# Optimization experiments

Measured on AMD Instinct MI355X. Metric: run time of the kernel, lower is better.

The kernel has to match this reference:

```python
import jax, jax.numpy as jnp
import numpy as np

N_T, N_I = 4096, 4096
TEXT_DIM, IMAGE_DIM, HIDDEN_DIM = 1024, 1024, 1024


def setup_inputs() -> dict:
    key = jax.random.key(0)
    ks = jax.random.split(key, 8)
    s_t = 1.0 / np.sqrt(TEXT_DIM)
    s_i = 1.0 / np.sqrt(IMAGE_DIM)
    return {
        "text_features": jax.random.normal(ks[0], (N_T, TEXT_DIM), jnp.float32),
        "image_features": jax.random.normal(ks[1], (N_I, IMAGE_DIM), jnp.float32),
        # nn.Linear params: weight [out, in], bias [out]
        "w_text": jax.random.uniform(ks[2], (HIDDEN_DIM, TEXT_DIM), jnp.float32, -s_t, s_t),
        "b_text": jax.random.uniform(ks[3], (HIDDEN_DIM,), jnp.float32, -s_t, s_t),
        "w_image": jax.random.uniform(ks[4], (HIDDEN_DIM, IMAGE_DIM), jnp.float32, -s_i, s_i),
        "b_image": jax.random.uniform(ks[5], (HIDDEN_DIM,), jnp.float32, -s_i, s_i),
        "scale_TI": jnp.ones((1,), jnp.float32),
        "scale_IT": jnp.ones((1,), jnp.float32),
    }


def reference(text_features, image_features, w_text, b_text, w_image, b_image, scale_TI, scale_IT):
    # linear projections to shared hidden space
    t = text_features @ w_text.T + b_text      # [N_t, H]
    i = image_features @ w_image.T + b_image   # [N_i, H]
    inv_sqrt_h = 1.0 / jnp.sqrt(jnp.asarray(HIDDEN_DIM, t.dtype))
    # text -> image attention: softmax over image axis, scaled post-softmax
    logits_TI = (t @ i.T) * inv_sqrt_h               # [N_t, N_i]
    attn_TI = jax.nn.softmax(logits_TI, axis=-1) * scale_TI
    # image -> text attention
    attn_IT = jax.nn.softmax(logits_TI.T, axis=-1) * scale_IT  # [N_i, N_t]
    text_attention_on_image = attn_TI @ image_features  # [N_t, image_dim]
    image_attention_on_text = attn_IT @ text_features   # [N_i, text_dim]
    return (text_attention_on_image, image_attention_on_text)
```

## Files before the change

kernel.cpp:

```cpp
#include <hip/hip_runtime.h>


typedef __bf16 bf16x8 __attribute__((ext_vector_type(8)));
typedef float f32x4 __attribute__((ext_vector_type(4)));

#define N_T 4096
#define N_I 4096
#define DIM 1024
#define TSS 136

__device__ __forceinline__ unsigned short f2bf(float f) {
    unsigned int u = __float_as_uint(f);
    u += 0x7fffu + ((u >> 16) & 1u);
    return (unsigned short)(u >> 16);
}

__device__ __forceinline__ void async_cp16(const unsigned short* g, unsigned short* l) {
    __builtin_amdgcn_global_load_lds(
        (const __attribute__((address_space(1))) unsigned int*)g,
        (__attribute__((address_space(3))) unsigned int*)l, 16, 0, 0);
}

__device__ __forceinline__ void stage_async(const unsigned short* __restrict__ src,
                                            int ld, int row0, int k0,
                                            unsigned short* lds, int t) {
    int r = t >> 2, c = (t & 3) << 3;
    const unsigned short* g = src + (size_t)(row0 + r) * ld + k0 + c;
    async_cp16(g, lds + r * 32 + c);
    async_cp16(g + (size_t)64 * ld, lds + (64 + r) * 32 + c);
}

__device__ __forceinline__ void mfma_step(const unsigned short* As,
                                          const unsigned short* Bs, f32x4 acc[4][4],
                                          int wrow, int wcol, int lane16, int quad) {
    bf16x8 a[4], b[4];
#pragma unroll
    for (int i = 0; i < 4; ++i) {
        a[i] = *(const bf16x8*)&As[(wrow + i * 16 + lane16) * 32 + quad * 8];
        b[i] = *(const bf16x8*)&Bs[(wcol + i * 16 + lane16) * 32 + quad * 8];
    }
#pragma unroll
    for (int i = 0; i < 4; ++i)
#pragma unroll
        for (int j = 0; j < 4; ++j)
            acc[i][j] = __builtin_amdgcn_mfma_f32_16x16x32_bf16(a[i], b[j], acc[i][j], 0, 0, 0);
}

__device__ __forceinline__ void tile_store(const unsigned short* sm,
                                           unsigned short* __restrict__ g, int ld,
                                           int row0, int col0, int tid) {
    int r = tid >> 1, h = (tid & 1) << 6;
    const unsigned short* src = sm + r * TSS + h;
    unsigned short* dst = g + (size_t)(row0 + r) * ld + col0 + h;
#pragma unroll
    for (int v = 0; v < 8; ++v)
        *(uint4*)(dst + v * 8) = *(const uint4*)(src + v * 8);
}

#define GEMM_IDX()                                               \
    int tid = threadIdx.x;                                       \
    int m0 = blockIdx.x * 128, n0 = blockIdx.y * 128;            \
    int lane = tid & 63, wave = tid >> 6;                        \
    int lane16 = lane & 15, quad = lane >> 4;                    \
    int wrow = (wave >> 1) * 64, wcol = (wave & 1) * 64;         \
    f32x4 acc[4][4];                                             \
    {                                                            \
        f32x4 z = {0.f, 0.f, 0.f, 0.f};                          \
        for (int i = 0; i < 4; ++i)                              \
            for (int j = 0; j < 4; ++j) acc[i][j] = z;           \
    }

__global__ void __launch_bounds__(256)
cvt_bf16_all(const float* __restrict__ t, const float* __restrict__ im,
             const float* __restrict__ wt, const float* __restrict__ wi,
             unsigned short* __restrict__ tb, unsigned short* __restrict__ imb,
             unsigned short* __restrict__ wtb, unsigned short* __restrict__ wib) {
    size_t i = (size_t)(blockIdx.x * 256 + threadIdx.x) * 8;
    const float* s;
    unsigned short* d;
    size_t off;
    if (i < 4194304)       { s = t;  d = tb;  off = i; }
    else if (i < 8388608)  { s = im; d = imb; off = i - 4194304; }
    else if (i < 9437184)  { s = wt; d = wtb; off = i - 8388608; }
    else                   { s = wi; d = wib; off = i - 9437184; }
    float4 f0 = *(const float4*)(s + off);
    float4 f1 = *(const float4*)(s + off + 4);
    uint4 o;
    o.x = (unsigned int)f2bf(f0.x) | ((unsigned int)f2bf(f0.y) << 16);
    o.y = (unsigned int)f2bf(f0.z) | ((unsigned int)f2bf(f0.w) << 16);
    o.z = (unsigned int)f2bf(f1.x) | ((unsigned int)f2bf(f1.y) << 16);
    o.w = (unsigned int)f2bf(f1.z) | ((unsigned int)f2bf(f1.w) << 16);
    *(uint4*)(d + off) = o;
}

__global__ void __launch_bounds__(256)
transpose_cvt2(const float* __restrict__ im, const float* __restrict__ tx,
               unsigned short* __restrict__ imgT, unsigned short* __restrict__ textT) {
    const float* in = blockIdx.z ? tx : im;
    unsigned short* out = blockIdx.z ? textT : imgT;
    __shared__ float tile[32][33];
    int c0 = blockIdx.x * 32, r0 = blockIdx.y * 32;
    int txi = threadIdx.x & 31, tyi = threadIdx.x >> 5;
#pragma unroll
    for (int i = tyi; i < 32; i += 8)
        tile[i][txi] = in[(size_t)(r0 + i) * DIM + c0 + txi];
    __syncthreads();
#pragma unroll
    for (int i = tyi; i < 32; i += 8)
        out[(size_t)(c0 + i) * N_T + r0 + txi] = f2bf(tile[txi][i]);
}

__global__ void __launch_bounds__(256, 2)
gemm_proj2(const unsigned short* __restrict__ Atx, const unsigned short* __restrict__ Wtx,
           const float* __restrict__ btx, unsigned short* __restrict__ Ctx,
           const unsigned short* __restrict__ Aim, const unsigned short* __restrict__ Wim,
           const float* __restrict__ bim, unsigned short* __restrict__ Cim) {
    __shared__ unsigned short As[128 * 32];
    __shared__ unsigned short Bs[128 * 32];
    int z = blockIdx.z;
    const unsigned short* A = z ? Aim : Atx;
    const unsigned short* W = z ? Wim : Wtx;
    const float* bias = z ? bim : btx;
    unsigned short* C = z ? Cim : Ctx;
    GEMM_IDX();
    for (int k0 = 0; k0 < DIM; k0 += 32) {
        stage_async(A, DIM, m0, k0, As, tid);
        stage_async(W, DIM, n0, k0, Bs, tid);
        __syncthreads();
        mfma_step(As, Bs, acc, wrow, wcol, lane16, quad);
        __syncthreads();
    }
#pragma unroll
    for (int j = 0; j < 4; ++j) {
        int col = n0 + wcol + j * 16 + lane16;
        float bv = bias[col];
#pragma unroll
        for (int i = 0; i < 4; ++i) {
            int rowb = m0 + wrow + i * 16 + quad * 4;
#pragma unroll
            for (int r = 0; r < 4; ++r)
                C[(size_t)(rowb + r) * DIM + col] = f2bf(acc[i][j][r] + bv);
        }
    }
}

__global__ void __launch_bounds__(256, 2)
gemm_logits_exp(const unsigned short* __restrict__ Tb,
                const unsigned short* __restrict__ Ib,
                unsigned short* __restrict__ P, unsigned short* __restrict__ PT,
                float* __restrict__ lT, float* __restrict__ lI) {
    __shared__ unsigned short smem[128 * TSS];
    unsigned short* As = smem;
    unsigned short* Bs = smem + 128 * 32;
    GEMM_IDX();
    for (int k0 = 0; k0 < DIM; k0 += 32) {
        stage_async(Tb, DIM, m0, k0, As, tid);
        stage_async(Ib, DIM, n0, k0, Bs, tid);
        __syncthreads();
        mfma_step(As, Bs, acc, wrow, wcol, lane16, quad);
        __syncthreads();
    }
#pragma unroll
    for (int i = 0; i < 4; ++i)
#pragma unroll
        for (int j = 0; j < 4; ++j)
#pragma unroll
            for (int r = 0; r < 4; ++r)
                acc[i][j][r] = __expf(acc[i][j][r] * 0.03125f);
#pragma unroll
    for (int i = 0; i < 4; ++i)
#pragma unroll
        for (int r = 0; r < 4; ++r) {
            float s = acc[i][0][r] + acc[i][1][r] + acc[i][2][r] + acc[i][3][r];
            s += __shfl_xor(s, 1); s += __shfl_xor(s, 2);
            s += __shfl_xor(s, 4); s += __shfl_xor(s, 8);
            if (lane16 == 0) atomicAdd(&lT[m0 + wrow + i * 16 + quad * 4 + r], s);
        }
#pragma unroll
    for (int j = 0; j < 4; ++j) {
        float s = 0.f;
#pragma unroll
        for (int i = 0; i < 4; ++i)
#pragma unroll
            for (int r = 0; r < 4; ++r) s += acc[i][j][r];
        s += __shfl_xor(s, 16); s += __shfl_xor(s, 32);
        if (quad == 0) atomicAdd(&lI[n0 + wcol + j * 16 + lane16], s);
    }
    __syncthreads();
#pragma unroll
    for (int i = 0; i < 4; ++i)
#pragma unroll
        for (int j = 0; j < 4; ++j)
#pragma unroll
            for (int r = 0; r < 4; ++r)
                smem[(wrow + i * 16 + quad * 4 + r) * TSS + wcol + j * 16 + lane16] =
                    f2bf(acc[i][j][r]);
    __syncthreads();
    tile_store(smem, P, N_I, m0, n0, tid);
    __syncthreads();
#pragma unroll
    for (int i = 0; i < 4; ++i)
#pragma unroll
        for (int j = 0; j < 4; ++j) {
            unsigned int lo = (unsigned int)f2bf(acc[i][j][0]) |
                              ((unsigned int)f2bf(acc[i][j][1]) << 16);
            unsigned int hi = (unsigned int)f2bf(acc[i][j][2]) |
                              ((unsigned int)f2bf(acc[i][j][3]) << 16);
            uint2 v; v.x = lo; v.y = hi;
            *(uint2*)&smem[(wcol + j * 16 + lane16) * TSS + wrow + i * 16 + quad * 4] = v;
        }
    __syncthreads();
    tile_store(smem, PT, N_T, n0, m0, tid);
}

__global__ void __launch_bounds__(512, 4)
gemm_attn2(const unsigned short* __restrict__ P, const unsigned short* __restrict__ imgT,
           const float* __restrict__ lT, const float* __restrict__ sTI,
           float* __restrict__ out0,
           const unsigned short* __restrict__ PT, const unsigned short* __restrict__ textT,
           const float* __restrict__ lI, const float* __restrict__ sIT,
           float* __restrict__ out1) {
    __shared__ unsigned short As[2][128 * 32];
    __shared__ unsigned short Bs[2][128 * 32];
    int which = blockIdx.z;
    const unsigned short* A = which ? PT : P;
    const unsigned short* Bt = which ? textT : imgT;
    const float* l = which ? lI : lT;
    const float* sp = which ? sIT : sTI;
    float* out = which ? out1 : out0;

    int tid = threadIdx.x;
    int half = tid >> 8;
    int t = tid & 255;
    int m0 = blockIdx.x * 128, n0 = blockIdx.y * 128;
    int lane = tid & 63;
    int wv = (tid >> 6) & 3;
    int lane16 = lane & 15, quad = lane >> 4;
    int wrow = (wv >> 1) * 64, wcol = (wv & 1) * 64;
    f32x4 acc[4][4];
    {
        f32x4 z = {0.f, 0.f, 0.f, 0.f};
        for (int i = 0; i < 4; ++i)
            for (int j = 0; j < 4; ++j) acc[i][j] = z;
    }

    int kbeg = half * 2048, kend = kbeg + 2048;
    for (int k0 = kbeg; k0 < kend; k0 += 32) {
        stage_async(A, 4096, m0, k0, As[half], t);
        stage_async(Bt, 4096, n0, k0, Bs[half], t);
        __syncthreads();
        mfma_step(As[half], Bs[half], acc, wrow, wcol, lane16, quad);
        __syncthreads();
    }

    float* red = (float*)As;
#pragma unroll
    for (int i = 0; i < 4; ++i) {
        __syncthreads();
        if (half) {
#pragma unroll
            for (int j = 0; j < 4; ++j)
                *(f32x4*)&red[wv * 1024 + lane * 16 + j * 4] = acc[i][j];
        }
        __syncthreads();
        if (!half) {
#pragma unroll
            for (int j = 0; j < 4; ++j)
                acc[i][j] += *(const f32x4*)&red[wv * 1024 + lane * 16 + j * 4];
        }
    }
    if (half) return;

    float sc = sp[0];
#pragma unroll
    for (int i = 0; i < 4; ++i) {
        int rowb = m0 + wrow + i * 16 + quad * 4;
        float fac[4];
#pragma unroll
        for (int r = 0; r < 4; ++r) fac[r] = sc / l[rowb + r];
#pragma unroll
        for (int j = 0; j < 4; ++j) {
            int col = n0 + wcol + j * 16 + lane16;
#pragma unroll
            for (int r = 0; r < 4; ++r)
                out[(size_t)(rowb + r) * DIM + col] = acc[i][j][r] * fac[r];
        }
    }
}

extern "C" void kernel_launch(void* const* d_in, const int* in_sizes, int n_in,
                              void* d_out, int out_size, void* d_ws, size_t ws_size,
                              hipStream_t stream) {
    const float* text = (const float*)d_in[0];
    const float* image = (const float*)d_in[1];
    const float* w_text = (const float*)d_in[2];
    const float* b_text = (const float*)d_in[3];
    const float* w_image = (const float*)d_in[4];
    const float* b_image = (const float*)d_in[5];
    const float* scale_TI = (const float*)d_in[6];
    const float* scale_IT = (const float*)d_in[7];
    float* out0 = (float*)d_out;
    float* out1 = out0 + (size_t)N_T * DIM;

    char* ws = (char*)d_ws;
    unsigned short* text_bf = (unsigned short*)(ws);
    unsigned short* image_bf = (unsigned short*)(ws + (8ull << 20));
    unsigned short* wt_bf = (unsigned short*)(ws + (16ull << 20));
    unsigned short* wi_bf = (unsigned short*)(ws + (18ull << 20));
    unsigned short* P = (unsigned short*)(ws);
    unsigned short* imgT = (unsigned short*)(ws + (32ull << 20));
    unsigned short* textT = (unsigned short*)(ws + (40ull << 20));
    unsigned short* t_bf = (unsigned short*)(ws + (48ull << 20));
    unsigned short* i_bf = (unsigned short*)(ws + (56ull << 20));
    unsigned short* PT = (unsigned short*)(ws + (64ull << 20));
    float* lT = (float*)(ws + (96ull << 20));
    float* lI = (float*)(ws + (96ull << 20) + 16384);

    hipMemsetAsync(lT, 0, 32768, stream);

    cvt_bf16_all<<<5120, 256, 0, stream>>>(text, image, w_text, w_image,
                                           text_bf, image_bf, wt_bf, wi_bf);
    transpose_cvt2<<<dim3(DIM / 32, N_T / 32, 2), 256, 0, stream>>>(image, text, imgT, textT);

    gemm_proj2<<<dim3(N_T / 128, DIM / 128, 2), 256, 0, stream>>>(
        text_bf, wt_bf, b_text, t_bf, image_bf, wi_bf, b_image, i_bf);

    gemm_logits_exp<<<dim3(N_T / 128, N_I / 128), 256, 0, stream>>>(t_bf, i_bf, P, PT, lT, lI);

    gemm_attn2<<<dim3(N_T / 128, DIM / 128, 2), 512, 0, stream>>>(
        P, imgT, lT, scale_TI, out0, PT, textT, lI, scale_IT, out1);
}
```

Before: 279.9 us.

## Fuse activation bf16 conversion into transpose and stage two K-slices per barrier

Result: faster. 270.8 us (-3.3%).

```diff
diff --git a/kernel.cpp b/kernel.cpp
--- a/kernel.cpp
+++ b/kernel.cpp
@@ -71,18 +71,14 @@
     }
 
 __global__ void __launch_bounds__(256)
-cvt_bf16_all(const float* __restrict__ t, const float* __restrict__ im,
-             const float* __restrict__ wt, const float* __restrict__ wi,
-             unsigned short* __restrict__ tb, unsigned short* __restrict__ imb,
-             unsigned short* __restrict__ wtb, unsigned short* __restrict__ wib) {
+cvt_w(const float* __restrict__ wt, const float* __restrict__ wi,
+      unsigned short* __restrict__ wtb, unsigned short* __restrict__ wib) {
     size_t i = (size_t)(blockIdx.x * 256 + threadIdx.x) * 8;
     const float* s;
     unsigned short* d;
     size_t off;
-    if (i < 4194304)       { s = t;  d = tb;  off = i; }
-    else if (i < 8388608)  { s = im; d = imb; off = i - 4194304; }
-    else if (i < 9437184)  { s = wt; d = wtb; off = i - 8388608; }
-    else                   { s = wi; d = wib; off = i - 9437184; }
+    if (i < 1048576) { s = wt; d = wtb; off = i; }
+    else             { s = wi; d = wib; off = i - 1048576; }
     float4 f0 = *(const float4*)(s + off);
     float4 f1 = *(const float4*)(s + off + 4);
     uint4 o;
@@ -94,40 +90,48 @@
 }
 
 __global__ void __launch_bounds__(256)
-transpose_cvt2(const float* __restrict__ im, const float* __restrict__ tx,
-               unsigned short* __restrict__ imgT, unsigned short* __restrict__ textT) {
+cvt_tr_fused(const float* __restrict__ im, const float* __restrict__ tx,
+             unsigned short* __restrict__ imb, unsigned short* __restrict__ txb,
+             unsigned short* __restrict__ imgT, unsigned short* __restrict__ textT) {
     const float* in = blockIdx.z ? tx : im;
-    unsigned short* out = blockIdx.z ? textT : imgT;
+    unsigned short* nb = blockIdx.z ? txb : imb;
+    unsigned short* tr = blockIdx.z ? textT : imgT;
     __shared__ float tile[32][33];
     int c0 = blockIdx.x * 32, r0 = blockIdx.y * 32;
     int txi = threadIdx.x & 31, tyi = threadIdx.x >> 5;
 #pragma unroll
+    for (int i = tyi; i < 32; i += 8) {
+        float v = in[(size_t)(r0 + i) * DIM + c0 + txi];
+        tile[i][txi] = v;
+        nb[(size_t)(r0 + i) * DIM + c0 + txi] = f2bf(v);
+    }
+    __syncthreads();
+#pragma unroll
     for (int i = tyi; i < 32; i += 8)
-        tile[i][txi] = in[(size_t)(r0 + i) * DIM + c0 + txi];
-    __syncthreads();
-#pragma unroll
-    for (int i = tyi; i < 32; i += 8)
-        out[(size_t)(c0 + i) * N_T + r0 + txi] = f2bf(tile[txi][i]);
-}
-
-__global__ void __launch_bounds__(256, 2)
+        tr[(size_t)(c0 + i) * N_T + r0 + txi] = f2bf(tile[txi][i]);
+}
+
+__global__ void __launch_bounds__(256, 4)
 gemm_proj2(const unsigned short* __restrict__ Atx, const unsigned short* __restrict__ Wtx,
            const float* __restrict__ btx, unsigned short* __restrict__ Ctx,
            const unsigned short* __restrict__ Aim, const unsigned short* __restrict__ Wim,
            const float* __restrict__ bim, unsigned short* __restrict__ Cim) {
-    __shared__ unsigned short As[128 * 32];
-    __shared__ unsigned short Bs[128 * 32];
+    __shared__ unsigned short As[2][128 * 32];
+    __shared__ unsigned short Bs[2][128 * 32];
     int z = blockIdx.z;
     const unsigned short* A = z ? Aim : Atx;
     const unsigned short* W = z ? Wim : Wtx;
     const float* bias = z ? bim : btx;
     unsigned short* C = z ? Cim : Ctx;
     GEMM_IDX();
-    for (int k0 = 0; k0 < DIM; k0 += 32) {
-        stage_async(A, DIM, m0, k0, As, tid);
-        stage_async(W, DIM, n0, k0, Bs, tid);
-        __syncthreads();
-        mfma_step(As, Bs, acc, wrow, wcol, lane16, quad);
+    for (int k0 = 0; k0 < DIM; k0 += 64) {
+        stage_async(A, DIM, m0, k0, As[0], tid);
+        stage_async(W, DIM, n0, k0, Bs[0], tid);
+        stage_async(A, DIM, m0, k0 + 32, As[1], tid);
+        stage_async(W, DIM, n0, k0 + 32, Bs[1], tid);
+        __syncthreads();
+        mfma_step(As[0], Bs[0], acc, wrow, wcol, lane16, quad);
+        mfma_step(As[1], Bs[1], acc, wrow, wcol, lane16, quad);
         __syncthreads();
     }
 #pragma unroll
@@ -144,20 +148,25 @@
     }
 }
 
-__global__ void __launch_bounds__(256, 2)
+__global__ void __launch_bounds__(256, 4)
 gemm_logits_exp(const unsigned short* __restrict__ Tb,
                 const unsigned short* __restrict__ Ib,
                 unsigned short* __restrict__ P, unsigned short* __restrict__ PT,
                 float* __restrict__ lT, float* __restrict__ lI) {
     __shared__ unsigned short smem[128 * TSS];
-    unsigned short* As = smem;
-    unsigned short* Bs = smem + 128 * 32;
+    unsigned short* As0 = smem;
+    unsigned short* Bs0 = smem + 4096;
+    unsigned short* As1 = smem + 8192;
+    unsigned short* Bs1 = smem + 12288;
     GEMM_IDX();
-    for (int k0 = 0; k0 < DIM; k0 += 32) {
-        stage_async(Tb, DIM, m0, k0, As, tid);
-        stage_async(Ib, DIM, n0, k0, Bs, tid);
-        __syncthreads();
-        mfma_step(As, Bs, acc, wrow, wcol, lane16, quad);
+    for (int k0 = 0; k0 < DIM; k0 += 64) {
+        stage_async(Tb, DIM, m0, k0, As0, tid);
+        stage_async(Ib, DIM, n0, k0, Bs0, tid);
+        stage_async(Tb, DIM, m0, k0 + 32, As1, tid);
+        stage_async(Ib, DIM, n0, k0 + 32, Bs1, tid);
+        __syncthreads();
+        mfma_step(As0, Bs0, acc, wrow, wcol, lane16, quad);
+        mfma_step(As1, Bs1, acc, wrow, wcol, lane16, quad);
         __syncthreads();
     }
 #pragma unroll
@@ -220,8 +229,8 @@
            const unsigned short* __restrict__ PT, const unsigned short* __restrict__ textT,
            const float* __restrict__ lI, const float* __restrict__ sIT,
            float* __restrict__ out1) {
-    __shared__ unsigned short As[2][128 * 32];
-    __shared__ unsigned short Bs[2][128 * 32];
+    __shared__ unsigned short As[2][2][128 * 32];
+    __shared__ unsigned short Bs[2][2][128 * 32];
     int which = blockIdx.z;
     const unsigned short* A = which ? PT : P;
     const unsigned short* Bt = which ? textT : imgT;
@@ -244,12 +253,15 @@
             for (int j = 0; j < 4; ++j) acc[i][j] = z;
     }
 
-    int kbeg = half * 2048, kend = kbeg + 2048;
-    for (int k0 = kbeg; k0 < kend; k0 += 32) {
-        stage_async(A, 4096, m0, k0, As[half], t);
-        stage_async(Bt, 4096, n0, k0, Bs[half], t);
-        __syncthreads();
-        mfma_step(As[half], Bs[half], acc, wrow, wcol, lane16, quad);
+    int kbeg = half * 2048;
+    for (int k0 = kbeg; k0 < kbeg + 2048; k0 += 64) {
+        stage_async(A, 4096, m0, k0, As[half][0], t);
+        stage_async(Bt, 4096, n0, k0, Bs[half][0], t);
+        stage_async(A, 4096, m0, k0 + 32, As[half][1], t);
+        stage_async(Bt, 4096, n0, k0 + 32, Bs[half][1], t);
+        __syncthreads();
+        mfma_step(As[half][0], Bs[half][0], acc, wrow, wcol, lane16, quad);
+        mfma_step(As[half][1], Bs[half][1], acc, wrow, wcol, lane16, quad);
         __syncthreads();
     }
 
@@ -318,9 +330,9 @@
 
     hipMemsetAsync(lT, 0, 32768, stream);
 
-    cvt_bf16_all<<<5120, 256, 0, stream>>>(text, image, w_text, w_image,
-                                           text_bf, image_bf, wt_bf, wi_bf);
-    transpose_cvt2<<<dim3(DIM / 32, N_T / 32, 2), 256, 0, stream>>>(image, text, imgT, textT);
+    cvt_w<<<1024, 256, 0, stream>>>(w_text, w_image, wt_bf, wi_bf);
+    cvt_tr_fused<<<dim3(DIM / 32, N_T / 32, 2), 256, 0, stream>>>(
+        image, text, image_bf, text_bf, imgT, textT);
 
     gemm_proj2<<<dim3(N_T / 128, DIM / 128, 2), 256, 0, stream>>>(
         text_bf, wt_bf, b_text, t_bf, image_bf, wi_bf, b_image, i_bf);
```
